# Performance work log

Measured on AMD Instinct MI355X. Metric: run time of the kernel, lower is better.

Reference implementation:

```python
import jax, jax.numpy as jnp
import numpy as np

C = 96          # num_features
G = 3           # deform / weight groups
K = 9           # 3x3 kernel taps
OFF_CH = G * 3 * K  # 81: offset-conv output channels


def conv3x3(x, w, b=None):
    out = jax.lax.conv_general_dilated(
        x, w, window_strides=(1, 1), padding=((1, 1), (1, 1)),
        dimension_numbers=('NCHW', 'OIHW', 'NCHW'))
    if b is not None:
        out = out + b[None, :, None, None]
    return out


def offset_gen(x):
    o1, o2, m = jnp.split(x, 3, axis=1)
    return jnp.concatenate([o1, o2], axis=1), jax.nn.sigmoid(m)


def dcn(x, offset, mask, w, b):
    # Modulated deformable conv (DCNv2): offset = [y-offsets (G*K ch), x-offsets (G*K ch)]
    N, Cx, H, W = x.shape
    Cg = Cx // G
    GK = G * K
    dy = offset[:, :GK].reshape(N, G, K, H, W)
    dx = offset[:, GK:].reshape(N, G, K, H, W)
    m = mask.reshape(N, G, K, H, W)
    ky = (jnp.arange(K) // 3 - 1).astype(x.dtype)
    kx = (jnp.arange(K) % 3 - 1).astype(x.dtype)
    # sampling positions: p = p0 + kernel_offset + learned_offset (stride 1, pad 1)
    py = dy + jnp.arange(H, dtype=x.dtype)[:, None] + ky[:, None, None]   # [N,G,K,H,W]
    px = dx + jnp.arange(W, dtype=x.dtype) + kx[:, None, None]
    y0 = jnp.floor(py)
    x0 = jnp.floor(px)
    xf = x.reshape(N, G, Cg, H * W)
    gather = jax.vmap(jax.vmap(lambda xg, ig: xg[:, ig]))  # ([Cg,HW],[KHW]) -> [Cg,KHW]
    val = jnp.zeros((N, G, Cg, K, H, W), x.dtype)
    for cy, cx in ((y0, x0), (y0, x0 + 1), (y0 + 1, x0), (y0 + 1, x0 + 1)):
        wgt = (1 - jnp.abs(py - cy)) * (1 - jnp.abs(px - cx))
        valid = (cy >= 0) & (cy <= H - 1) & (cx >= 0) & (cx <= W - 1)
        iy = jnp.clip(cy, 0, H - 1).astype(jnp.int32)
        ix = jnp.clip(cx, 0, W - 1).astype(jnp.int32)
        idx = (iy * W + ix).reshape(N, G, K * H * W)
        g = gather(xf, idx).reshape(N, G, Cg, K, H, W)
        val = val + g * (wgt * valid.astype(x.dtype))[:, :, None]
    val = val * m[:, :, None]                       # modulation
    wg = w.reshape(G, Cx // G, Cg, K)               # grouped weight [G, Cout/G, Cin/G, K]
    out = jnp.einsum('ngckhw,gock->ngohw', val, wg).reshape(N, Cx, H, W)
    return out + b[None, :, None, None]


def setup_inputs() -> dict:
    key = jax.random.key(0)
    ks = jax.random.split(key, 16)
    B, H, W = 2, 128, 128
    d = {
        'X1': jax.random.normal(ks[0], (B, C, H, W), jnp.float32),
        'X2': jax.random.normal(ks[1], (B, C, H, W), jnp.float32),
        'w_bot': jax.random.normal(ks[2], (C, 2 * C, 3, 3), jnp.float32) * 0.02,
    }
    for i in range(4):
        d[f'w_off{i+1}'] = jax.random.normal(ks[3 + i], (OFF_CH, C, 3, 3), jnp.float32) * 0.02
        d[f'w_d{i+1}'] = jax.random.normal(ks[7 + i], (C, C // G, 3, 3), jnp.float32) * 0.05
        d[f'b_d{i+1}'] = jax.random.normal(ks[11 + i], (C,), jnp.float32) * 0.01
    return d


def reference(X1, X2, w_bot, w_off1, w_off2, w_off3, w_off4,
              w_d1, b_d1, w_d2, b_d2, w_d3, b_d3, w_d4, b_d4):
    B, Cx, H, W = X1.shape
    # frames: f0 = cat(X1, X1), f1 = cat(X1, X2) along channels, flattened to (B*2, 2C, H, W)
    feat = jnp.stack([jnp.concatenate([X1, X1], axis=1),
                      jnp.concatenate([X1, X2], axis=1)], axis=1)
    feat = feat.reshape(B * 2, 2 * Cx, H, W)
    feat = conv3x3(feat, w_bot)
    for w_off, w_d, b_d in ((w_off1, w_d1, b_d1), (w_off2, w_d2, b_d2),
                            (w_off3, w_d3, b_d3), (w_off4, w_d4, b_d4)):
        off, m = offset_gen(conv3x3(feat, w_off))
        feat = dcn(feat, off, m, w_d, b_d)
    return feat[1:2]


if __name__ == '__main__':
    out = reference(**setup_inputs())
    print(out.shape)
```

## Files before the change

### kernel.cpp

```cpp
#include <hip/hip_runtime.h>

#define HW 16384
#define RSB 130

typedef short short8 __attribute__((ext_vector_type(8)));
typedef float f32x4 __attribute__((ext_vector_type(4)));
typedef unsigned short ushort8v __attribute__((ext_vector_type(8)));

__device__ __forceinline__ float b2f(unsigned short u) {
    return __uint_as_float(((unsigned)u) << 16);
}
__device__ __forceinline__ unsigned short f2b(float f) {
    unsigned u = __float_as_uint(f);
    return (unsigned short)((u + 0x7fffu + ((u >> 16) & 1u)) >> 16);
}

__global__ __launch_bounds__(256) void prep_all(
    const float* __restrict__ X1, const float* __restrict__ X2,
    const float* __restrict__ w_bot,
    const float* __restrict__ wo0, const float* __restrict__ wo1,
    const float* __restrict__ wo2, const float* __restrict__ wo3,
    const float* __restrict__ wd0, const float* __restrict__ wd1,
    const float* __restrict__ wd2, const float* __restrict__ wd3,
    unsigned short* __restrict__ wBbot, unsigned short* __restrict__ wBoff,
    unsigned short* __restrict__ wdB,  unsigned short* __restrict__ in_nhwc,
    unsigned short* __restrict__ featA, unsigned short* __restrict__ featB) {
    const int N0 = 165888, N1 = N0 + 331776, N2 = N1 + 110592,
              N3 = N2 + 393216, N4 = N3 + 24768;
    for (int idx = blockIdx.x * 256 + threadIdx.x; idx < N4; idx += 131072) {
        if (idx < N0) {
            int i = idx;
            int v = i & 7, lane = (i >> 3) & 63, t = i >> 9;
            int kc = t % 6; t /= 6;
            int tap = t % 9, nt = t / 9;
            int oc = nt * 16 + (lane & 15), cin = kc * 32 + (lane >> 4) * 8 + v;
            wBbot[i] = f2b(oc < 96 ? w_bot[(oc * 192 + cin) * 9 + tap] : 0.f);
        } else if (idx < N1) {
            int j = idx - N0;
            int l = j / 82944, i = j - l * 82944;
            const float* w = l == 0 ? wo0 : l == 1 ? wo1 : l == 2 ? wo2 : wo3;
            int v = i & 7, lane = (i >> 3) & 63, t = i >> 9;
            int kc = t % 3; t /= 3;
            int tap = t % 9, nt = t / 9;
            int oc = nt * 16 + (lane & 15), cin = kc * 32 + (lane >> 4) * 8 + v;
            wBoff[j] = f2b(oc < 81 ? w[(oc * 96 + cin) * 9 + tap] : 0.f);
        } else if (idx < N2) {
            int j = idx - N1;
            int l = j / 27648, i = j - l * 27648;
            const float* w = l == 0 ? wd0 : l == 1 ? wd1 : l == 2 ? wd2 : wd3;
            int v = i & 7, lane = (i >> 3) & 63, t = i >> 9;
            int nt = t & 1; t >>= 1;
            int tap = t % 9, g = t / 9;
            int oc = nt * 16 + (lane & 15), c = (lane >> 4) * 8 + v;
            wdB[j] = f2b(w[((g * 32 + oc) * 32 + c) * 9 + tap]);
        } else if (idx < N3) {
            int j = idx - N2;
            int cb = j >> 14, p = j & (HW - 1);
            int ch = cb * 8;
            int y = p >> 7, x = p & 127;
            ushort8v o;
#pragma unroll
            for (int q = 0; q < 8; ++q) {
                int c = ch + q;
                float v = (c < 96) ? X1[c * HW + p] : X2[(c - 96) * HW + p];
                o[q] = f2b(v);
            }
            *(ushort8v*)(in_nhwc + (size_t)((y + 1) * RSB + (x + 1)) * 192 + ch) = o;
        } else {
            int j = idx - N3;
            int bp = j / 48, c8 = j - bp * 48;
            int y, x;
            if (bp < 130)      { y = 0;   x = bp; }
            else if (bp < 260) { y = 129; x = bp - 130; }
            else { int t2 = bp - 260; y = 1 + (t2 >> 1); x = (t2 & 1) ? 129 : 0; }
            size_t pix = (size_t)y * RSB + x;
            ushort8v z = {0, 0, 0, 0, 0, 0, 0, 0};
            if (c8 < 24)      *(ushort8v*)(in_nhwc + pix * 192 + c8 * 8) = z;
            else if (c8 < 36) *(ushort8v*)(featA + pix * 96 + (c8 - 24) * 8) = z;
            else              *(ushort8v*)(featB + pix * 96 + (c8 - 36) * 8) = z;
        }
    }
}

__global__ __launch_bounds__(192) void conv_bot(const unsigned short* __restrict__ in,
                                                const unsigned short* __restrict__ wB,
                                                unsigned short* __restrict__ outb) {
    const int tid = threadIdx.x;
    const int lane = tid & 63;
    const int w = tid >> 6;
    const int col = lane & 15, klane = lane >> 4;
    const int pb = ((blockIdx.x & 7) << 7) + (blockIdx.x >> 3);
    const int pbase = pb * 16;
    const int p = pbase + col;
    const int y = p >> 7, x = p & 127;
    const unsigned short* arow = in + (size_t)((y + 1) * RSB + (x + 1)) * 192 + klane * 8;
    const int nt0 = 2 * w;
    const unsigned short* wb = wB + (size_t)nt0 * 9 * 6 * 512 + lane * 8;

    f32x4 a0 = {0.f, 0.f, 0.f, 0.f};
    f32x4 a1 = {0.f, 0.f, 0.f, 0.f};
#pragma unroll
    for (int tap = 0; tap < 9; ++tap) {
        const unsigned short* at = arow + ((tap / 3 - 1) * RSB + (tap % 3 - 1)) * 192;
#pragma unroll
        for (int kc = 0; kc < 6; ++kc) {
            short8 a  = *(const short8*)(at + kc * 32);
            short8 b0 = *(const short8*)(wb + ((0 * 9 + tap) * 6 + kc) * 512);
            short8 b1 = *(const short8*)(wb + ((1 * 9 + tap) * 6 + kc) * 512);
            a0 = __builtin_amdgcn_mfma_f32_16x16x32_bf16(a, b0, a0, 0, 0, 0);
            a1 = __builtin_amdgcn_mfma_f32_16x16x32_bf16(a, b1, a1, 0, 0, 0);
        }
    }
#pragma unroll
    for (int r = 0; r < 4; ++r) {
        int pr = pbase + klane * 4 + r;
        int yy = pr >> 7, xx = pr & 127;
        size_t base = (size_t)((yy + 1) * RSB + (xx + 1)) * 96;
        outb[base + (nt0 + 0) * 16 + col] = f2b(a0[r]);
        outb[base + (nt0 + 1) * 16 + col] = f2b(a1[r]);
    }
}

__global__ __launch_bounds__(192) void offdcn_kernel(
    const unsigned short* __restrict__ feat,
    const unsigned short* __restrict__ wBoff,
    const unsigned short* __restrict__ wdB,
    const float* __restrict__ b_d,
    void* __restrict__ outp, int last) {
    __shared__ float s_off[16][97];

    const int tid = threadIdx.x;
    const int lane = tid & 63;
    const int w = tid >> 6;
    const int col = lane & 15, klane = lane >> 4;
    const int pb = ((blockIdx.x & 7) << 7) + (blockIdx.x >> 3);
    const int P0 = pb * 16;
    const int p = P0 + col;
    const int y = p >> 7, x = p & 127;

    {
        const unsigned short* arow = feat + (size_t)((y + 1) * RSB + (x + 1)) * 96 + klane * 8;
        const int nt0 = 2 * w;
        const unsigned short* wb = wBoff + (size_t)nt0 * 9 * 3 * 512 + lane * 8;

        f32x4 a0 = {0.f, 0.f, 0.f, 0.f};
        f32x4 a1 = {0.f, 0.f, 0.f, 0.f};
#pragma unroll
        for (int tap = 0; tap < 9; ++tap) {
            const unsigned short* at = arow + ((tap / 3 - 1) * RSB + (tap % 3 - 1)) * 96;
#pragma unroll
            for (int kc = 0; kc < 3; ++kc) {
                short8 a  = *(const short8*)(at + kc * 32);
                short8 b0 = *(const short8*)(wb + ((0 * 9 + tap) * 3 + kc) * 512);
                short8 b1 = *(const short8*)(wb + ((1 * 9 + tap) * 3 + kc) * 512);
                a0 = __builtin_amdgcn_mfma_f32_16x16x32_bf16(a, b0, a0, 0, 0, 0);
                a1 = __builtin_amdgcn_mfma_f32_16x16x32_bf16(a, b1, a1, 0, 0, 0);
            }
        }
#pragma unroll
        for (int r = 0; r < 4; ++r) {
            int pl = klane * 4 + r;
            s_off[pl][(nt0 + 0) * 16 + col] = a0[r];
            s_off[pl][(nt0 + 1) * 16 + col] = a1[r];
        }
    }
    __syncthreads();

    {
        const int g = w;
        const int coct = klane * 8;

        const unsigned short* fgc = feat + g * 32 + coct;
        const unsigned short* wb = wdB + (size_t)g * 9 * 2 * 512 + lane * 8;

        int adr[9][4];
        float wgt[9][4];
#pragma unroll
        for (int k = 0; k < 9; ++k) {
            float dy = s_off[col][g * 9 + k];
            float dx = s_off[col][27 + g * 9 + k];
            float mr = s_off[col][54 + g * 9 + k];
            float m = 1.f / (1.f + __expf(-mr));

            float py = dy + (float)y + (float)(k / 3 - 1);
            float px = dx + (float)x + (float)(k % 3 - 1);
            float y0f = floorf(py), x0f = floorf(px);
            float fy = py - y0f, fx = px - x0f;
            float gy = 1.f - fy, gx = 1.f - fx;

            int py0 = (int)y0f + 1, px0 = (int)x0f + 1;
            int iy0 = min(max(py0, 0), 129);
            int iy1 = min(max(py0 + 1, 0), 129);
            int ix0 = min(max(px0, 0), 129);
            int ix1 = min(max(px0 + 1, 0), 129);

            wgt[k][0] = gy * gx * m;
            wgt[k][1] = gy * fx * m;
            wgt[k][2] = fy * gx * m;
            wgt[k][3] = fy * fx * m;

            adr[k][0] = iy0 * RSB + ix0;
            adr[k][1] = iy0 * RSB + ix1;
            adr[k][2] = iy1 * RSB + ix0;
            adr[k][3] = iy1 * RSB + ix1;
        }

        f32x4 acc0 = {0.f, 0.f, 0.f, 0.f};
        f32x4 acc1 = {0.f, 0.f, 0.f, 0.f};

        ushort8v ga[4], gb[4], gc[4];
#define LDG(buf, kk) { \
        buf[0] = *(const ushort8v*)(fgc + (size_t)adr[kk][0] * 96); \
        buf[1] = *(const ushort8v*)(fgc + (size_t)adr[kk][1] * 96); \
        buf[2] = *(const ushort8v*)(fgc + (size_t)adr[kk][2] * 96); \
        buf[3] = *(const ushort8v*)(fgc + (size_t)adr[kk][3] * 96); }
#define CMP(buf, kk) { \
        short8 a; \
        _Pragma("unroll") for (int j = 0; j < 8; ++j) { \
            float val = fmaf(wgt[kk][0], b2f(buf[0][j]), \
                        fmaf(wgt[kk][1], b2f(buf[1][j]), \
                        fmaf(wgt[kk][2], b2f(buf[2][j]), \
                             wgt[kk][3] * b2f(buf[3][j])))); \
            a[j] = (short)f2b(val); } \
        short8 b0 = *(const short8*)(wb + ((kk) * 2 + 0) * 512); \
        short8 b1 = *(const short8*)(wb + ((kk) * 2 + 1) * 512); \
        acc0 = __builtin_amdgcn_mfma_f32_16x16x32_bf16(a, b0, acc0, 0, 0, 0); \
        acc1 = __builtin_amdgcn_mfma_f32_16x16x32_bf16(a, b1, acc1, 0, 0, 0); }

        LDG(ga, 0); LDG(gb, 1); LDG(gc, 2);
        CMP(ga, 0); LDG(ga, 3);
        CMP(gb, 1); LDG(gb, 4);
        CMP(gc, 2); LDG(gc, 5);
        CMP(ga, 3); LDG(ga, 6);
        CMP(gb, 4); LDG(gb, 7);
        CMP(gc, 5); LDG(gc, 8);
        CMP(ga, 6); CMP(gb, 7); CMP(gc, 8);
#undef LDG
#undef CMP

#pragma unroll
        for (int r = 0; r < 4; ++r) {
            int pr = P0 + klane * 4 + r;
            int ch0 = g * 32 + col, ch1 = g * 32 + 16 + col;
            float o0 = acc0[r] + b_d[ch0];
            float o1 = acc1[r] + b_d[ch1];
            if (!last) {
                int yy = pr >> 7, xx = pr & 127;
                unsigned short* fo = (unsigned short*)outp;
                size_t base = (size_t)((yy + 1) * RSB + (xx + 1)) * 96;
                fo[base + ch0] = f2b(o0);
                fo[base + ch1] = f2b(o1);
            } else {
                float* fo = (float*)outp;
                fo[(size_t)ch0 * HW + pr] = o0;
                fo[(size_t)ch1 * HW + pr] = o1;
            }
        }
    }
}

extern "C" void kernel_launch(void* const* d_in, const int* in_sizes, int n_in,
                              void* d_out, int out_size, void* d_ws, size_t ws_size,
                              hipStream_t stream) {
    const float* X1    = (const float*)d_in[0];
    const float* X2    = (const float*)d_in[1];
    const float* w_bot = (const float*)d_in[2];
    const float* wo0 = (const float*)d_in[3],  *wo1 = (const float*)d_in[6],
               *wo2 = (const float*)d_in[9],  *wo3 = (const float*)d_in[12];
    const float* wd0 = (const float*)d_in[4],  *wd1 = (const float*)d_in[7],
               *wd2 = (const float*)d_in[10], *wd3 = (const float*)d_in[13];
    const float* bd[4] = {(const float*)d_in[5], (const float*)d_in[8],
                          (const float*)d_in[11], (const float*)d_in[14]};

    unsigned short* in_nhwc = (unsigned short*)d_ws;
    unsigned short* featA   = in_nhwc + 3244800;
    unsigned short* featB   = featA + 1622400;
    unsigned short* wBbot   = featB + 1622400;
    unsigned short* wBoff   = wBbot + 165888;
    unsigned short* wdB     = wBoff + 4 * 82944;

    prep_all<<<512, 256, 0, stream>>>(X1, X2, w_bot, wo0, wo1, wo2, wo3,
                                      wd0, wd1, wd2, wd3,
                                      wBbot, wBoff, wdB, in_nhwc, featA, featB);
    conv_bot<<<1024, 192, 0, stream>>>(in_nhwc, wBbot, featA);

    unsigned short* cur = featA;
    unsigned short* nxt = featB;
    for (int it = 0; it < 4; ++it) {
        void* outp = (it == 3) ? d_out : (void*)nxt;
        offdcn_kernel<<<1024, 192, 0, stream>>>(cur, wBoff + it * 82944,
                                                wdB + it * 27648, bd[it],
                                                outp, it == 3 ? 1 : 0);
        unsigned short* t = cur; cur = nxt; nxt = t;
    }
}
```

Before: 127.2 us.

## Process 64 pixels per block to reuse weight fragments across four M-tiles

conv_bot and offdcn_kernel now handle four 16-pixel M-fragments per block instead of one, so each loaded B-weight fragment feeds four MFMAs and the grid shrinks from 1024 to 256 blocks. The DCN stage loops over the four fragments serially, with the offset tile held in a larger shared array. This cuts redundant weight loads from global memory and cache. In exchange it raises register pressure (eight accumulators) and leaves only 256 blocks, which may underfill the GPU's compute units and reduce latency hiding.

```diff
diff --git a/kernel.cpp b/kernel.cpp
--- a/kernel.cpp
+++ b/kernel.cpp
@@ -89,36 +89,51 @@
     const int lane = tid & 63;
     const int w = tid >> 6;
     const int col = lane & 15, klane = lane >> 4;
-    const int pb = ((blockIdx.x & 7) << 7) + (blockIdx.x >> 3);
-    const int pbase = pb * 16;
-    const int p = pbase + col;
-    const int y = p >> 7, x = p & 127;
-    const unsigned short* arow = in + (size_t)((y + 1) * RSB + (x + 1)) * 192 + klane * 8;
+    const int pb = ((blockIdx.x & 7) << 5) + (blockIdx.x >> 3);
+    const int P0 = pb * 64;
+
+    const unsigned short* arow[4];
+#pragma unroll
+    for (int mf = 0; mf < 4; ++mf) {
+        int p = P0 + mf * 16 + col;
+        int y = p >> 7, x = p & 127;
+        arow[mf] = in + (size_t)((y + 1) * RSB + (x + 1)) * 192 + klane * 8;
+    }
     const int nt0 = 2 * w;
     const unsigned short* wb = wB + (size_t)nt0 * 9 * 6 * 512 + lane * 8;
 
-    f32x4 a0 = {0.f, 0.f, 0.f, 0.f};
-    f32x4 a1 = {0.f, 0.f, 0.f, 0.f};
+    f32x4 acc[4][2];
+#pragma unroll
+    for (int mf = 0; mf < 4; ++mf)
+#pragma unroll
+        for (int n = 0; n < 2; ++n) acc[mf][n] = (f32x4){0.f, 0.f, 0.f, 0.f};
+
 #pragma unroll
     for (int tap = 0; tap < 9; ++tap) {
-        const unsigned short* at = arow + ((tap / 3 - 1) * RSB + (tap % 3 - 1)) * 192;
+        const int toff = ((tap / 3 - 1) * RSB + (tap % 3 - 1)) * 192;
 #pragma unroll
         for (int kc = 0; kc < 6; ++kc) {
-            short8 a  = *(const short8*)(at + kc * 32);
             short8 b0 = *(const short8*)(wb + ((0 * 9 + tap) * 6 + kc) * 512);
             short8 b1 = *(const short8*)(wb + ((1 * 9 + tap) * 6 + kc) * 512);
-            a0 = __builtin_amdgcn_mfma_f32_16x16x32_bf16(a, b0, a0, 0, 0, 0);
-            a1 = __builtin_amdgcn_mfma_f32_16x16x32_bf16(a, b1, a1, 0, 0, 0);
-        }
-    }
-#pragma unroll
-    for (int r = 0; r < 4; ++r) {
-        int pr = pbase + klane * 4 + r;
-        int yy = pr >> 7, xx = pr & 127;
-        size_t base = (size_t)((yy + 1) * RSB + (xx + 1)) * 96;
-        outb[base + (nt0 + 0) * 16 + col] = f2b(a0[r]);
-        outb[base + (nt0 + 1) * 16 + col] = f2b(a1[r]);
-    }
+#pragma unroll
+            for (int mf = 0; mf < 4; ++mf) {
+                short8 a = *(const short8*)(arow[mf] + toff + kc * 32);
+                acc[mf][0] = __builtin_amdgcn_mfma_f32_16x16x32_bf16(a, b0, acc[mf][0], 0, 0, 0);
+                acc[mf][1] = __builtin_amdgcn_mfma_f32_16x16x32_bf16(a, b1, acc[mf][1], 0, 0, 0);
+            }
+        }
+    }
+
+#pragma unroll
+    for (int mf = 0; mf < 4; ++mf)
+#pragma unroll
+        for (int r = 0; r < 4; ++r) {
+            int pr = P0 + mf * 16 + klane * 4 + r;
+            int yy = pr >> 7, xx = pr & 127;
+            size_t base = (size_t)((yy + 1) * RSB + (xx + 1)) * 96;
+            outb[base + (nt0 + 0) * 16 + col] = f2b(acc[mf][0][r]);
+            outb[base + (nt0 + 1) * 16 + col] = f2b(acc[mf][1][r]);
+        }
 }
 
 __global__ __launch_bounds__(192) void offdcn_kernel(
@@ -127,133 +142,152 @@
     const unsigned short* __restrict__ wdB,
     const float* __restrict__ b_d,
     void* __restrict__ outp, int last) {
-    __shared__ float s_off[16][97];
+    __shared__ float s_off[64][97];
 
     const int tid = threadIdx.x;
     const int lane = tid & 63;
     const int w = tid >> 6;
     const int col = lane & 15, klane = lane >> 4;
-    const int pb = ((blockIdx.x & 7) << 7) + (blockIdx.x >> 3);
-    const int P0 = pb * 16;
-    const int p = P0 + col;
-    const int y = p >> 7, x = p & 127;
+    const int pb = ((blockIdx.x & 7) << 5) + (blockIdx.x >> 3);
+    const int P0 = pb * 64;
 
     {
-        const unsigned short* arow = feat + (size_t)((y + 1) * RSB + (x + 1)) * 96 + klane * 8;
+        const unsigned short* arow[4];
+#pragma unroll
+        for (int mf = 0; mf < 4; ++mf) {
+            int p = P0 + mf * 16 + col;
+            int y = p >> 7, x = p & 127;
+            arow[mf] = feat + (size_t)((y + 1) * RSB + (x + 1)) * 96 + klane * 8;
+        }
         const int nt0 = 2 * w;
         const unsigned short* wb = wBoff + (size_t)nt0 * 9 * 3 * 512 + lane * 8;
 
-        f32x4 a0 = {0.f, 0.f, 0.f, 0.f};
-        f32x4 a1 = {0.f, 0.f, 0.f, 0.f};
+        f32x4 acc[4][2];
+#pragma unroll
+        for (int mf = 0; mf < 4; ++mf)
+#pragma unroll
+            for (int n = 0; n < 2; ++n) acc[mf][n] = (f32x4){0.f, 0.f, 0.f, 0.f};
+
 #pragma unroll
         for (int tap = 0; tap < 9; ++tap) {
-            const unsigned short* at = arow + ((tap / 3 - 1) * RSB + (tap % 3 - 1)) * 96;
+            const int toff = ((tap / 3 - 1) * RSB + (tap % 3 - 1)) * 96;
 #pragma unroll
             for (int kc = 0; kc < 3; ++kc) {
-                short8 a  = *(const short8*)(at + kc * 32);
                 short8 b0 = *(const short8*)(wb + ((0 * 9 + tap) * 3 + kc) * 512);
                 short8 b1 = *(const short8*)(wb + ((1 * 9 + tap) * 3 + kc) * 512);
-                a0 = __builtin_amdgcn_mfma_f32_16x16x32_bf16(a, b0, a0, 0, 0, 0);
-                a1 = __builtin_amdgcn_mfma_f32_16x16x32_bf16(a, b1, a1, 0, 0, 0);
-            }
-        }
-#pragma unroll
-        for (int r = 0; r < 4; ++r) {
-            int pl = klane * 4 + r;
-            s_off[pl][(nt0 + 0) * 16 + col] = a0[r];
-            s_off[pl][(nt0 + 1) * 16 + col] = a1[r];
-        }
+#pragma unroll
+                for (int mf = 0; mf < 4; ++mf) {
+                    short8 a = *(const short8*)(arow[mf] + toff + kc * 32);
+                    acc[mf][0] = __builtin_amdgcn_mfma_f32_16x16x32_bf16(a, b0, acc[mf][0], 0, 0, 0);
+                    acc[mf][1] = __builtin_amdgcn_mfma_f32_16x16x32_bf16(a, b1, acc[mf][1], 0, 0, 0);
+                }
+            }
+        }
+#pragma unroll
+        for (int mf = 0; mf < 4; ++mf)
+#pragma unroll
+            for (int r = 0; r < 4; ++r) {
+                int pl = mf * 16 + klane * 4 + r;
+                s_off[pl][(nt0 + 0) * 16 + col] = acc[mf][0][r];
+                s_off[pl][(nt0 + 1) * 16 + col] = acc[mf][1][r];
+            }
     }
     __syncthreads();
 
     {
         const int g = w;
         const int coct = klane * 8;
-
         const unsigned short* fgc = feat + g * 32 + coct;
         const unsigned short* wb = wdB + (size_t)g * 9 * 2 * 512 + lane * 8;
 
-        int adr[9][4];
-        float wgt[9][4];
-#pragma unroll
-        for (int k = 0; k < 9; ++k) {
-            float dy = s_off[col][g * 9 + k];
-            float dx = s_off[col][27 + g * 9 + k];
-            float mr = s_off[col][54 + g * 9 + k];
-            float m = 1.f / (1.f + __expf(-mr));
-
-            float py = dy + (float)y + (float)(k / 3 - 1);
-            float px = dx + (float)x + (float)(k % 3 - 1);
-            float y0f = floorf(py), x0f = floorf(px);
-            float fy = py - y0f, fx = px - x0f;
-            float gy = 1.f - fy, gx = 1.f - fx;
-
-            int py0 = (int)y0f + 1, px0 = (int)x0f + 1;
-            int iy0 = min(max(py0, 0), 129);
-            int iy1 = min(max(py0 + 1, 0), 129);
-            int ix0 = min(max(px0, 0), 129);
-            int ix1 = min(max(px0 + 1, 0), 129);
-
-            wgt[k][0] = gy * gx * m;
-            wgt[k][1] = gy * fx * m;
-            wgt[k][2] = fy * gx * m;
-            wgt[k][3] = fy * fx * m;
-
-            adr[k][0] = iy0 * RSB + ix0;
-            adr[k][1] = iy0 * RSB + ix1;
-            adr[k][2] = iy1 * RSB + ix0;
-            adr[k][3] = iy1 * RSB + ix1;
-        }
-
-        f32x4 acc0 = {0.f, 0.f, 0.f, 0.f};
-        f32x4 acc1 = {0.f, 0.f, 0.f, 0.f};
-
-        ushort8v ga[4], gb[4], gc[4];
+#pragma unroll 1
+        for (int mf = 0; mf < 4; ++mf) {
+            const int p = P0 + mf * 16 + col;
+            const int y = p >> 7, x = p & 127;
+            const int pl = mf * 16 + col;
+
+            int adr[9][4];
+            float wgt[9][4];
+#pragma unroll
+            for (int k = 0; k < 9; ++k) {
+                float dy = s_off[pl][g * 9 + k];
+                float dx = s_off[pl][27 + g * 9 + k];
+                float mr = s_off[pl][54 + g * 9 + k];
+                float m = 1.f / (1.f + __expf(-mr));
+
+                float py = dy + (float)y + (float)(k / 3 - 1);
+                float px = dx + (float)x + (float)(k % 3 - 1);
+                float y0f = floorf(py), x0f = floorf(px);
+                float fy = py - y0f, fx = px - x0f;
+                float gy = 1.f - fy, gx = 1.f - fx;
+
+                int py0 = (int)y0f + 1, px0 = (int)x0f + 1;
+                int iy0 = min(max(py0, 0), 129);
+                int iy1 = min(max(py0 + 1, 0), 129);
+                int ix0 = min(max(px0, 0), 129);
+                int ix1 = min(max(px0 + 1, 0), 129);
+
+                wgt[k][0] = gy * gx * m;
+                wgt[k][1] = gy * fx * m;
+                wgt[k][2] = fy * gx * m;
+                wgt[k][3] = fy * fx * m;
+
+                adr[k][0] = iy0 * RSB + ix0;
+                adr[k][1] = iy0 * RSB + ix1;
+                adr[k][2] = iy1 * RSB + ix0;
+                adr[k][3] = iy1 * RSB + ix1;
+            }
+
+            f32x4 acc0 = {0.f, 0.f, 0.f, 0.f};
+            f32x4 acc1 = {0.f, 0.f, 0.f, 0.f};
+
+            ushort8v ga[4], gb[4], gc[4];
 #define LDG(buf, kk) { \
-        buf[0] = *(const ushort8v*)(fgc + (size_t)adr[kk][0] * 96); \
-        buf[1] = *(const ushort8v*)(fgc + (size_t)adr[kk][1] * 96); \
-        buf[2] = *(const ushort8v*)(fgc + (size_t)adr[kk][2] * 96); \
-        buf[3] = *(const ushort8v*)(fgc + (size_t)adr[kk][3] * 96); }
+            buf[0] = *(const ushort8v*)(fgc + (size_t)adr[kk][0] * 96); \
+            buf[1] = *(const ushort8v*)(fgc + (size_t)adr[kk][1] * 96); \
+            buf[2] = *(const ushort8v*)(fgc + (size_t)adr[kk][2] * 96); \
+            buf[3] = *(const ushort8v*)(fgc + (size_t)adr[kk][3] * 96); }
 #define CMP(buf, kk) { \
-        short8 a; \
-        _Pragma("unroll") for (int j = 0; j < 8; ++j) { \
-            float val = fmaf(wgt[kk][0], b2f(buf[0][j]), \
-                        fmaf(wgt[kk][1], b2f(buf[1][j]), \
-                        fmaf(wgt[kk][2], b2f(buf[2][j]), \
-                             wgt[kk][3] * b2f(buf[3][j])))); \
-            a[j] = (short)f2b(val); } \
-        short8 b0 = *(const short8*)(wb + ((kk) * 2 + 0) * 512); \
-        short8 b1 = *(const short8*)(wb + ((kk) * 2 + 1) * 512); \
-        acc0 = __builtin_amdgcn_mfma_f32_16x16x32_bf16(a, b0, acc0, 0, 0, 0); \
-        acc1 = __builtin_amdgcn_mfma_f32_16x16x32_bf16(a, b1, acc1, 0, 0, 0); }
-
-        LDG(ga, 0); LDG(gb, 1); LDG(gc, 2);
-        CMP(ga, 0); LDG(ga, 3);
-        CMP(gb, 1); LDG(gb, 4);
-        CMP(gc, 2); LDG(gc, 5);
-        CMP(ga, 3); LDG(ga, 6);
-        CMP(gb, 4); LDG(gb, 7);
-        CMP(gc, 5); LDG(gc, 8);
-        CMP(ga, 6); CMP(gb, 7); CMP(gc, 8);
+            short8 a; \
+            _Pragma("unroll") for (int j = 0; j < 8; ++j) { \
+                float val = fmaf(wgt[kk][0], b2f(buf[0][j]), \
+                            fmaf(wgt[kk][1], b2f(buf[1][j]), \
+                            fmaf(wgt[kk][2], b2f(buf[2][j]), \
+                                 wgt[kk][3] * b2f(buf[3][j])))); \
+                a[j] = (short)f2b(val); } \
+            short8 b0 = *(const short8*)(wb + ((kk) * 2 + 0) * 512); \
+            short8 b1 = *(const short8*)(wb + ((kk) * 2 + 1) * 512); \
+            acc0 = __builtin_amdgcn_mfma_f32_16x16x32_bf16(a, b0, acc0, 0, 0, 0); \
+            acc1 = __builtin_amdgcn_mfma_f32_16x16x32_bf16(a, b1, acc1, 0, 0, 0); }
+
+            LDG(ga, 0); LDG(gb, 1); LDG(gc, 2);
+            CMP(ga, 0); LDG(ga, 3);
+            CMP(gb, 1); LDG(gb, 4);
+            CMP(gc, 2); LDG(gc, 5);
+            CMP(ga, 3); LDG(ga, 6);
+            CMP(gb, 4); LDG(gb, 7);
+            CMP(gc, 5); LDG(gc, 8);
+            CMP(ga, 6); CMP(gb, 7); CMP(gc, 8);
 #undef LDG
 #undef CMP
 
 #pragma unroll
-        for (int r = 0; r < 4; ++r) {
-            int pr = P0 + klane * 4 + r;
-            int ch0 = g * 32 + col, ch1 = g * 32 + 16 + col;
-            float o0 = acc0[r] + b_d[ch0];
-            float o1 = acc1[r] + b_d[ch1];
-            if (!last) {
-                int yy = pr >> 7, xx = pr & 127;
-                unsigned short* fo = (unsigned short*)outp;
-                size_t base = (size_t)((yy + 1) * RSB + (xx + 1)) * 96;
-                fo[base + ch0] = f2b(o0);
-                fo[base + ch1] = f2b(o1);
-            } else {
-                float* fo = (float*)outp;
-                fo[(size_t)ch0 * HW + pr] = o0;
-                fo[(size_t)ch1 * HW + pr] = o1;
+            for (int r = 0; r < 4; ++r) {
+                int pr = P0 + mf * 16 + klane * 4 + r;
+                int ch0 = g * 32 + col, ch1 = g * 32 + 16 + col;
+                float o0 = acc0[r] + b_d[ch0];
+                float o1 = acc1[r] + b_d[ch1];
+                if (!last) {
+                    int yy = pr >> 7, xx = pr & 127;
+                    unsigned short* fo = (unsigned short*)outp;
+                    size_t base = (size_t)((yy + 1) * RSB + (xx + 1)) * 96;
+                    fo[base + ch0] = f2b(o0);
+                    fo[base + ch1] = f2b(o1);
+                } else {
+                    float* fo = (float*)outp;
+                    fo[(size_t)ch0 * HW + pr] = o0;
+                    fo[(size_t)ch1 * HW + pr] = o1;
+                }
             }
         }
     }
@@ -282,15 +316,15 @@
     prep_all<<<512, 256, 0, stream>>>(X1, X2, w_bot, wo0, wo1, wo2, wo3,
                                       wd0, wd1, wd2, wd3,
                                       wBbot, wBoff, wdB, in_nhwc, featA, featB);
-    conv_bot<<<1024, 192, 0, stream>>>(in_nhwc, wBbot, featA);
+    conv_bot<<<256, 192, 0, stream>>>(in_nhwc, wBbot, featA);
 
     unsigned short* cur = featA;
     unsigned short* nxt = featB;
     for (int it = 0; it < 4; ++it) {
         void* outp = (it == 3) ? d_out : (void*)nxt;
-        offdcn_kernel<<<1024, 192, 0, stream>>>(cur, wBoff + it * 82944,
-                                                wdB + it * 27648, bd[it],
-                                                outp, it == 3 ? 1 : 0);
+        offdcn_kernel<<<256, 192, 0, stream>>>(cur, wBoff + it * 82944,
+                                               wdB + it * 27648, bd[it],
+                                               outp, it == 3 ? 1 : 0);
         unsigned short* t = cur; cur = nxt; nxt = t;
     }
 }
```

Measured after the change: 151.6 us. 1.19x slower.
